# Kernel optimization log

Measured on AMD Instinct MI355X. Metric: run time of the kernel, lower is better.

## Reference

```python
import jax, jax.numpy as jnp
import numpy as np

B, T, C, H = 2, 2048, 1024, 16
HD = C // H  # head dim = 64


def setup_inputs() -> dict:
    key = jax.random.key(0)
    k0, k1, k2 = jax.random.split(key, 3)
    x = jax.random.normal(k0, (B, T, C), jnp.float32)
    W_attn = jax.random.normal(k1, (C, 3 * C), jnp.float32) * 0.02
    b_attn = jnp.zeros((3 * C,), jnp.float32)
    W_proj = jax.random.normal(k2, (C, C), jnp.float32) * 0.02
    b_proj = jnp.zeros((C,), jnp.float32)
    # rope: (1,1,T,HD//2,2,2) stack of 2x2 rotation matrices [[cos,-sin],[sin,cos]]
    inv_freq = 1.0 / (10000.0 ** (jnp.arange(0, HD, 2, dtype=jnp.float32) / HD))
    ang = jnp.arange(T, dtype=jnp.float32)[:, None] * inv_freq[None, :]  # (T, HD//2)
    cos, sin = jnp.cos(ang), jnp.sin(ang)
    rope = jnp.stack([jnp.stack([cos, -sin], -1), jnp.stack([sin, cos], -1)], -2)
    rope = rope[None, None]  # (1,1,T,HD//2,2,2)
    return dict(x=x, W_attn=W_attn, b_attn=b_attn, W_proj=W_proj, b_proj=b_proj, rope=rope)


def reference(x, W_attn, b_attn, W_proj, b_proj, rope):
    Bv, Tv, Cv = x.shape
    Hd = Cv // H
    qkv = x @ W_attn + b_attn                      # (B,T,3C) fused QKV proj
    q, k, v = jnp.split(qkv, 3, axis=-1)

    def heads(t):
        return t.reshape(Bv, Tv, H, Hd).transpose(0, 2, 1, 3)  # (B,H,T,Hd)

    q, k, v = heads(q), heads(k), heads(v)

    cos = rope[..., 0, 0][..., None]               # (1,1,T,Hd//2,1)
    sin = rope[..., 1, 0][..., None]

    def rot(t):
        tr = t.reshape(Bv, H, Tv, Hd // 2, 2)
        xr, yr = tr[..., 0:1], tr[..., 1:2]
        out = jnp.concatenate([xr * cos - yr * sin, xr * sin + yr * cos], axis=-1)
        return out.reshape(Bv, H, Tv, Hd)

    q, k = rot(q), rot(k)

    scale = 1.0 / np.sqrt(Hd).astype(np.float32)
    att = jnp.einsum('bhqd,bhkd->bhqk', q, k) * scale
    mask = jnp.tril(jnp.ones((Tv, Tv), dtype=bool))  # causal
    att = jnp.where(mask[None, None], att, -jnp.inf)
    att = jax.nn.softmax(att, axis=-1)
    y = jnp.einsum('bhqk,bhkd->bhqd', att, v)
    y = y.transpose(0, 2, 1, 3).reshape(Bv, Tv, Cv)
    return y @ W_proj + b_proj
```

## Files before the change

kernel.cpp:

```cpp
#include <hip/hip_runtime.h>
#include <hip/hip_bf16.h>

typedef __attribute__((ext_vector_type(8))) short short8;
typedef __attribute__((ext_vector_type(4))) short short4b;
typedef __attribute__((ext_vector_type(4))) float f32x4;
typedef __attribute__((ext_vector_type(16))) float f32x16;
typedef __attribute__((ext_vector_type(4))) unsigned u32x4;

static constexpr int Bb = 2, Tt = 2048, Cc = 1024, Hh = 16;
static constexpr int BT = Bb * Tt;
static constexpr int N1 = 3 * Cc;

__device__ __forceinline__ unsigned short f2b(float f) {
  union { float f; unsigned u; } v; v.f = f;
  unsigned r = v.u + 0x7fffu + ((v.u >> 16) & 1u);
  return (unsigned short)(r >> 16);
}
__device__ __forceinline__ float b2f(short s) {
  union { unsigned u; float f; } v; v.u = ((unsigned)(unsigned short)s) << 16;
  return v.f;
}

__global__ __launch_bounds__(256) void k_cast(const float* __restrict__ in,
                                              unsigned short* __restrict__ out, int n) {
  int i = (blockIdx.x * 256 + threadIdx.x) * 8;
  if (i >= n) return;
  float4 a = *reinterpret_cast<const float4*>(in + i);
  float4 b = *reinterpret_cast<const float4*>(in + i + 4);
  short8 o;
  o[0] = f2b(a.x); o[1] = f2b(a.y); o[2] = f2b(a.z); o[3] = f2b(a.w);
  o[4] = f2b(b.x); o[5] = f2b(b.y); o[6] = f2b(b.z); o[7] = f2b(b.w);
  *reinterpret_cast<short8*>(out + i) = o;
}

__global__ __launch_bounds__(256) void k_tcast(const float* __restrict__ in,
                                               unsigned short* __restrict__ out,
                                               int R, int Ccol) {
  __shared__ float tile[32][33];
  int cb = blockIdx.x * 32, rb = blockIdx.y * 32;
  int tx = threadIdx.x & 31, ty = threadIdx.x >> 5;
  for (int i = 0; i < 32; i += 8)
    tile[ty + i][tx] = in[(size_t)(rb + ty + i) * Ccol + cb + tx];
  __syncthreads();
  for (int i = 0; i < 32; i += 8)
    out[(size_t)(cb + ty + i) * R + rb + tx] = f2b(tile[tx][ty + i]);
}

template <int NF, int OUT_BF16>
__global__ __launch_bounds__(512, 2)
void k_gemm8(const unsigned short* __restrict__ A, const unsigned short* __restrict__ Bt,
             const float* __restrict__ bias, void* __restrict__ Cout,
             int M, int N, int K) {
  constexpr int BN = NF * 64;
  constexpr int ASZ = 256 * 64;
  constexpr int BSZ = BN * 64;
  constexpr int STRIDE = ASZ + BSZ;
  extern __shared__ unsigned short lds[];
  const int tid = threadIdx.x, lane = tid & 63, w = tid >> 6;
  const int wm = w >> 2, wn = w & 3;
  const int l15 = lane & 15, l4 = lane >> 4;
  int nbx = gridDim.x;
  int lin = blockIdx.y * nbx + blockIdx.x;
  int cpx = (nbx * gridDim.y) >> 3;
  lin = (lin & 7) * cpx + (lin >> 3);
  const int mb = lin / nbx, nb = lin % nbx;
  const size_t arow0 = (size_t)mb * 256;
  const size_t brow0 = (size_t)nb * BN;

  const int srow = lane >> 3;
  const int scol = (((lane & 7) * 16) ^ (srow << 4)) >> 1;
  auto stage = [&](int buf, int k0) {
    unsigned short* Ab = lds + buf * STRIDE;
    unsigned short* Bb = Ab + ASZ;
#pragma unroll
    for (int i = 0; i < 4; i++) {
      int c = w + 8 * i;
      const unsigned short* g = A + (arow0 + c * 8 + srow) * (size_t)K + k0 + scol;
      __builtin_amdgcn_global_load_lds((const __attribute__((address_space(1))) void*)g,
          (__attribute__((address_space(3))) void*)(Ab + c * 512), 16, 0, 0);
    }
#pragma unroll
    for (int i = 0; i < NF; i++) {
      int c = w + 8 * i;
      const unsigned short* g = Bt + (brow0 + c * 8 + srow) * (size_t)K + k0 + scol;
      __builtin_amdgcn_global_load_lds((const __attribute__((address_space(1))) void*)g,
          (__attribute__((address_space(3))) void*)(Bb + c * 512), 16, 0, 0);
    }
  };

  f32x4 acc[8][NF] = {};
  const int NK = K >> 6;

  stage(0, 0);
  asm volatile("s_waitcnt vmcnt(0)" ::: "memory");
  asm volatile("s_barrier" ::: "memory");

  for (int kt = 0; kt < NK; kt++) {
    int buf = kt & 1;
    if (kt + 1 < NK) stage(buf ^ 1, (kt + 1) << 6);
    const unsigned short* Ab = lds + buf * STRIDE;
    const unsigned short* Bb = Ab + ASZ;
    short8 af[8][2];
#pragma unroll
    for (int p = 0; p < NF; p++) {
      if (p == 0) {
#pragma unroll
        for (int m = 0; m < 8; m++) {
          int ra = wm * 128 + m * 16 + l15;
#pragma unroll
          for (int kk = 0; kk < 2; kk++) {
            int cb = (kk * 64 + l4 * 16) ^ ((ra & 7) << 4);
            af[m][kk] = *reinterpret_cast<const short8*>(Ab + ra * 64 + (cb >> 1));
          }
        }
      }
      short8 bfr[2];
      int rb = wn * (NF * 16) + p * 16 + l15;
#pragma unroll
      for (int kk = 0; kk < 2; kk++) {
        int cb = (kk * 64 + l4 * 16) ^ ((rb & 7) << 4);
        bfr[kk] = *reinterpret_cast<const short8*>(Bb + rb * 64 + (cb >> 1));
      }
      asm volatile("s_barrier" ::: "memory");
      asm volatile("s_waitcnt lgkmcnt(0)" ::: "memory");
      __builtin_amdgcn_sched_barrier(0);
      __builtin_amdgcn_s_setprio(1);
#pragma unroll
      for (int m = 0; m < 8; m++) {
        acc[m][p] = __builtin_amdgcn_mfma_f32_16x16x32_bf16(af[m][0], bfr[0], acc[m][p], 0, 0, 0);
        acc[m][p] = __builtin_amdgcn_mfma_f32_16x16x32_bf16(af[m][1], bfr[1], acc[m][p], 0, 0, 0);
      }
      __builtin_amdgcn_s_setprio(0);
      if (p == NF - 1)
        asm volatile("s_waitcnt vmcnt(0)" ::: "memory");
      asm volatile("s_barrier" ::: "memory");
    }
  }

#pragma unroll
  for (int m = 0; m < 8; m++) {
#pragma unroll
    for (int n = 0; n < NF; n++) {
      int ccol = nb * BN + wn * (NF * 16) + n * 16 + l15;
      float bv = bias[ccol];
#pragma unroll
      for (int j = 0; j < 4; j++) {
        int r = mb * 256 + wm * 128 + m * 16 + l4 * 4 + j;
        float v = acc[m][n][j] + bv;
        if (OUT_BF16)
          ((unsigned short*)Cout)[(size_t)r * N + ccol] = f2b(v);
        else
          ((float*)Cout)[(size_t)r * N + ccol] = v;
      }
    }
  }
}

__global__ __launch_bounds__(256)
void k_rope(const unsigned short* __restrict__ qkv, const float* __restrict__ rope,
            unsigned short* __restrict__ Qs, unsigned short* __restrict__ Ks,
            unsigned short* __restrict__ Vt) {
  __shared__ unsigned short vt_l[64][72];
  const float QS = 0.125f * 1.44269504f;
  int bid = blockIdx.x;
  int tb = bid & 31, h = (bid >> 5) & 15, b = bid >> 9;
  int tid = threadIdx.x;
#pragma unroll
  for (int r = 0; r < 2; r++) {
    int e = (r * 256 + tid) * 8;
    int tl = e >> 6, d = e & 63;
    int t = tb * 64 + tl;
    const unsigned short* rowp = qkv + (size_t)(b * Tt + t) * 3072 + h * 64 + d;
    short8 qv = *reinterpret_cast<const short8*>(rowp);
    short8 kv = *reinterpret_cast<const short8*>(rowp + 1024);
    short8 vv = *reinterpret_cast<const short8*>(rowp + 2048);
    short8 qo, ko;
#pragma unroll
    for (int p = 0; p < 4; p++) {
      int j = (d >> 1) + p;
      float4 rv = *reinterpret_cast<const float4*>(rope + ((size_t)t * 32 + j) * 4);
      float xq = b2f(qv[2 * p]), yq = b2f(qv[2 * p + 1]);
      float xk = b2f(kv[2 * p]), yk = b2f(kv[2 * p + 1]);
      qo[2 * p]     = (short)f2b((xq * rv.x + yq * rv.y) * QS);
      qo[2 * p + 1] = (short)f2b((xq * rv.z + yq * rv.w) * QS);
      ko[2 * p]     = (short)f2b(xk * rv.x + yk * rv.y);
      ko[2 * p + 1] = (short)f2b(xk * rv.z + yk * rv.w);
    }
    size_t qdst = ((size_t)(b * 16 + h) * Tt + t) * 64 + d;
    *reinterpret_cast<short8*>(Qs + qdst) = qo;
    *reinterpret_cast<short8*>(Ks + qdst) = ko;
#pragma unroll
    for (int i2 = 0; i2 < 8; i2++) vt_l[d + i2][tl] = (unsigned short)vv[i2];
  }
  __syncthreads();
#pragma unroll
  for (int r = 0; r < 2; r++) {
    int e = (r * 256 + tid) * 8;
    int dl = e >> 6, tl = e & 63;
    short8 o = *reinterpret_cast<const short8*>(&vt_l[dl][tl]);
    *reinterpret_cast<short8*>(Vt + ((size_t)(b * 16 + h) * 64 + dl) * Tt + tb * 64 + tl) = o;
  }
}

__device__ __forceinline__ float tmax16(const f32x16& v) {
  float a0 = fmaxf(v[0], v[1]),   a1 = fmaxf(v[2], v[3]);
  float a2 = fmaxf(v[4], v[5]),   a3 = fmaxf(v[6], v[7]);
  float a4 = fmaxf(v[8], v[9]),   a5 = fmaxf(v[10], v[11]);
  float a6 = fmaxf(v[12], v[13]), a7 = fmaxf(v[14], v[15]);
  float b0 = fmaxf(a0, a1), b1 = fmaxf(a2, a3), b2 = fmaxf(a4, a5), b3 = fmaxf(a6, a7);
  return fmaxf(fmaxf(b0, b1), fmaxf(b2, b3));
}

template <bool DIAG>
__device__ __forceinline__ void attn_tile128(
    const unsigned short* Kl, const unsigned short* Vl,
    int w, int l31, int hi, const short8 qf[4],
    float& m_run, float& l_run, f32x16 oacc[2]) {
  const int ktmax = DIAG ? w : 3;
  f32x16 s[4];
#pragma unroll
  for (int kt = 0; kt < 4; kt++) {
    if (kt > ktmax) continue;
    f32x16 acc = {};
    int rk = kt * 32 + l31;
    int sw = (rk & 7) << 4;
    const unsigned short* krow = Kl + rk * 64;
#pragma unroll
    for (int kk = 0; kk < 4; kk++) {
      short8 kf = *reinterpret_cast<const short8*>(krow + (((kk * 32 + hi * 16) ^ sw) >> 1));
      acc = __builtin_amdgcn_mfma_f32_32x32x16_bf16(kf, qf[kk], acc, 0, 0, 0);
    }
    if (DIAG && kt == w) {
#pragma unroll
      for (int r = 0; r < 16; r++) {
        int e = (r & 3) + 8 * (r >> 2) + 4 * hi;
        if (e > l31) acc[r] = -1e30f;
      }
    }
    s[kt] = acc;
  }
  float km[4];
#pragma unroll
  for (int kt = 0; kt < 4; kt++) km[kt] = (kt <= ktmax) ? tmax16(s[kt]) : -1e30f;
  float mx = fmaxf(fmaxf(km[0], km[1]), fmaxf(km[2], km[3]));
  mx = fmaxf(mx, __shfl_xor(mx, 32));
  float nm = fmaxf(m_run, mx);
  float fsc = __builtin_amdgcn_exp2f(m_run - nm);
  m_run = nm;
#pragma unroll
  for (int dt = 0; dt < 2; dt++)
#pragma unroll
    for (int r = 0; r < 16; r++) oacc[dt][r] *= fsc;

  float kps[4] = {0.f, 0.f, 0.f, 0.f};
#pragma unroll
  for (int kt = 0; kt < 4; kt++) {
    if (kt > ktmax) continue;
    float p[16];
#pragma unroll
    for (int r = 0; r < 16; r++) p[r] = __builtin_amdgcn_exp2f(s[kt][r] - nm);
    float s0 = (p[0] + p[1]) + (p[2] + p[3]);
    float s1 = (p[4] + p[5]) + (p[6] + p[7]);
    float s2 = (p[8] + p[9]) + (p[10] + p[11]);
    float s3 = (p[12] + p[13]) + (p[14] + p[15]);
    kps[kt] = (s0 + s1) + (s2 + s3);
    unsigned P[8];
#pragma unroll
    for (int i = 0; i < 8; i++) {
      unsigned lo = (__builtin_bit_cast(unsigned, p[2 * i]) + 0x8000u) >> 16;
      unsigned h2 = (__builtin_bit_cast(unsigned, p[2 * i + 1]) + 0x8000u) & 0xffff0000u;
      P[i] = lo | h2;
    }
    unsigned Y0 = (unsigned)__shfl_xor((int)(hi ? P[0] : P[2]), 32);
    unsigned Y1 = (unsigned)__shfl_xor((int)(hi ? P[1] : P[3]), 32);
    unsigned Y2 = (unsigned)__shfl_xor((int)(hi ? P[4] : P[6]), 32);
    unsigned Y3 = (unsigned)__shfl_xor((int)(hi ? P[5] : P[7]), 32);
    u32x4 c0 = hi ? u32x4{Y0, Y1, P[2], P[3]} : u32x4{P[0], P[1], Y0, Y1};
    u32x4 c1 = hi ? u32x4{Y2, Y3, P[6], P[7]} : u32x4{P[4], P[5], Y2, Y3};
    short8 pf0 = __builtin_bit_cast(short8, c0);
    short8 pf1 = __builtin_bit_cast(short8, c1);
#pragma unroll
    for (int dt = 0; dt < 2; dt++) {
      int d = dt * 32 + l31;
      int sv = (d & 15) << 4;
      const unsigned short* vrow = Vl + d * 128;
      short8 vf0 = *reinterpret_cast<const short8*>(vrow + (((kt * 64 + hi * 16) ^ sv) >> 1));
      short8 vf1 = *reinterpret_cast<const short8*>(vrow + (((kt * 64 + 32 + hi * 16) ^ sv) >> 1));
      oacc[dt] = __builtin_amdgcn_mfma_f32_32x32x16_bf16(vf0, pf0, oacc[dt], 0, 0, 0);
      oacc[dt] = __builtin_amdgcn_mfma_f32_32x32x16_bf16(vf1, pf1, oacc[dt], 0, 0, 0);
    }
  }
  float psum = (kps[0] + kps[1]) + (kps[2] + kps[3]);
  psum += __shfl_xor(psum, 32);
  l_run = l_run * fsc + psum;
}

__global__ __launch_bounds__(256)
void k_attn(const unsigned short* __restrict__ Qs, const unsigned short* __restrict__ Ks,
            const unsigned short* __restrict__ Vt, unsigned short* __restrict__ Y) {
  __shared__ unsigned short lds[32768];
  int tid = threadIdx.x, lane = tid & 63, w = tid >> 6;
  int s = blockIdx.x;
  int half = s >> 8;
  int p = s & 255;
  int bh = p >> 3;
  int j = p & 7;
  int qb = half ? j : 15 - j;
  int b = bh >> 4, h = bh & 15;
  int l31 = lane & 31, hi = lane >> 5;
  int qw0 = qb * 128 + w * 32;
  const unsigned short* Qb = Qs + (size_t)bh * Tt * 64;
  const unsigned short* Kb = Ks + (size_t)bh * Tt * 64;
  const unsigned short* Vb = Vt + (size_t)bh * 64 * Tt;

  auto stage = [&](int buf, int kv0) {
    unsigned short* Kbuf = lds + buf * 8192;
    unsigned short* Vbuf = lds + 16384 + buf * 8192;
    int krow = lane >> 3;
    int kcolb = ((lane & 7) * 16) ^ ((krow & 7) << 4);
#pragma unroll
    for (int cc = 0; cc < 4; cc++) {
      int c = w + cc * 4;
      const unsigned short* gk = Kb + (size_t)(kv0 + c * 8 + krow) * 64 + (kcolb >> 1);
      __builtin_amdgcn_global_load_lds((const __attribute__((address_space(1))) void*)gk,
          (__attribute__((address_space(3))) void*)(Kbuf + c * 512), 16, 0, 0);
      int vr = c * 4 + (lane >> 4);
      int vcolb = ((lane & 15) * 16) ^ ((vr & 15) << 4);
      const unsigned short* gv = Vb + (size_t)vr * Tt + kv0 + (vcolb >> 1);
      __builtin_amdgcn_global_load_lds((const __attribute__((address_space(1))) void*)gv,
          (__attribute__((address_space(3))) void*)(Vbuf + c * 512), 16, 0, 0);
    }
  };

  short8 qf[4];
#pragma unroll
  for (int kk = 0; kk < 4; kk++)
    qf[kk] = *reinterpret_cast<const short8*>(Qb + (size_t)(qw0 + l31) * 64 + kk * 16 + hi * 8);

  float m_run = -1e30f, l_run = 0.f;
  f32x16 oacc[2] = {};
  const int nt = qb + 1;

  stage(0, 0);
  __syncthreads();
  int cur = 0;
  for (int it = 0; it < nt - 1; ++it) {
    stage(cur ^ 1, (it + 1) * 128);
    attn_tile128<false>(lds + cur * 8192, lds + 16384 + cur * 8192,
                        w, l31, hi, qf, m_run, l_run, oacc);
    __syncthreads();
    cur ^= 1;
  }
  attn_tile128<true>(lds + cur * 8192, lds + 16384 + cur * 8192,
                     w, l31, hi, qf, m_run, l_run, oacc);

  float inv = 1.0f / l_run;
  int t = qw0 + l31;
  unsigned short* yrow = Y + ((size_t)b * Tt + t) * Cc + h * 64;
#pragma unroll
  for (int dt = 0; dt < 2; dt++)
#pragma unroll
    for (int q4 = 0; q4 < 4; q4++) {
      short4b o;
#pragma unroll
      for (int jj = 0; jj < 4; jj++) o[jj] = (short)f2b(oacc[dt][q4 * 4 + jj] * inv);
      *reinterpret_cast<short4b*>(yrow + dt * 32 + q4 * 8 + hi * 4) = o;
    }
}

extern "C" void kernel_launch(void* const* d_in, const int* in_sizes, int n_in,
                              void* d_out, int out_size, void* d_ws, size_t ws_size,
                              hipStream_t stream) {
  (void)in_sizes; (void)n_in; (void)out_size; (void)ws_size;
  const float* x      = (const float*)d_in[0];
  const float* W_attn = (const float*)d_in[1];
  const float* b_attn = (const float*)d_in[2];
  const float* W_proj = (const float*)d_in[3];
  const float* b_proj = (const float*)d_in[4];
  const float* rope   = (const float*)d_in[5];
  float* out = (float*)d_out;

  char* ws = (char*)d_ws;
  unsigned short* xb  = (unsigned short*)(ws);
  unsigned short* WaT = (unsigned short*)(ws + (8u << 20));
  unsigned short* WpT = (unsigned short*)(ws + (14u << 20));
  unsigned short* qkv = (unsigned short*)(ws + (16u << 20));
  unsigned short* Qs  = (unsigned short*)(ws + (40u << 20));
  unsigned short* Ks  = (unsigned short*)(ws + (48u << 20));
  unsigned short* Vt  = (unsigned short*)(ws + (56u << 20));
  unsigned short* Yb  = (unsigned short*)(ws + (64u << 20));

  constexpr int LDS_QKV  = (256 + 192) * 64 * 2 * 2;
  constexpr int LDS_PROJ = (256 + 128) * 64 * 2 * 2;
  (void)hipFuncSetAttribute(reinterpret_cast<const void*>(&k_gemm8<3, 1>),
                            hipFuncAttributeMaxDynamicSharedMemorySize, LDS_QKV);
  (void)hipFuncSetAttribute(reinterpret_cast<const void*>(&k_gemm8<2, 0>),
                            hipFuncAttributeMaxDynamicSharedMemorySize, LDS_PROJ);

  k_cast<<<2048, 256, 0, stream>>>(x, xb, BT * Cc);
  k_tcast<<<dim3(N1 / 32, Cc / 32), 256, 0, stream>>>(W_attn, WaT, Cc, N1);
  k_tcast<<<dim3(Cc / 32, Cc / 32), 256, 0, stream>>>(W_proj, WpT, Cc, Cc);
  k_gemm8<3, 1><<<dim3(N1 / 192, BT / 256), 512, LDS_QKV, stream>>>(xb, WaT, b_attn, qkv, BT, N1, Cc);
  k_rope<<<Bb * Hh * (Tt / 64), 256, 0, stream>>>(qkv, rope, Qs, Ks, Vt);
  k_attn<<<Bb * Hh * (Tt / 128), 256, 0, stream>>>(Qs, Ks, Vt, Yb);
  k_gemm8<2, 0><<<dim3(Cc / 128, BT / 256), 512, LDS_PROJ, stream>>>(Yb, WpT, b_proj, out, BT, Cc, Cc);
}
```

Before: 121.9 us.

## Fuse RoPE, scaling and head scatter into QKV GEMM epilogue; remap attention blocks per XCD

Removes the separate rope kernel and the intermediate qkv buffer. The QKV GEMM epilogue now applies bias, RoPE (pairing lanes via shuffle) and the softmax scale, then writes Q/K in head-major layout and V transposed. This avoids a full round trip of the qkv tensor through memory and one launch, at the cost of scattered 2-byte stores in the epilogue. Attention block indexing is also remapped so each XCD handles a fixed set of heads, with a heavy-first causal ordering, to improve L2 locality.

```diff
diff --git a/kernel.cpp b/kernel.cpp
--- a/kernel.cpp
+++ b/kernel.cpp
@@ -10,6 +10,7 @@
 static constexpr int Bb = 2, Tt = 2048, Cc = 1024, Hh = 16;
 static constexpr int BT = Bb * Tt;
 static constexpr int N1 = 3 * Cc;
+static constexpr float QS = 0.125f * 1.44269504f;
 
 __device__ __forceinline__ unsigned short f2b(float f) {
   union { float f; unsigned u; } v; v.f = f;
@@ -46,10 +47,12 @@
     out[(size_t)(cb + ty + i) * R + rb + tx] = f2b(tile[tx][ty + i]);
 }
 
-template <int NF, int OUT_BF16>
+template <int NF, int EPI>
 __global__ __launch_bounds__(512, 2)
 void k_gemm8(const unsigned short* __restrict__ A, const unsigned short* __restrict__ Bt,
              const float* __restrict__ bias, void* __restrict__ Cout,
+             const float* __restrict__ rope, unsigned short* __restrict__ Qs,
+             unsigned short* __restrict__ Ks, unsigned short* __restrict__ Vt,
              int M, int N, int K) {
   constexpr int BN = NF * 64;
   constexpr int ASZ = 256 * 64;
@@ -141,64 +144,45 @@
   for (int m = 0; m < 8; m++) {
 #pragma unroll
     for (int n = 0; n < NF; n++) {
-      int ccol = nb * BN + wn * (NF * 16) + n * 16 + l15;
-      float bv = bias[ccol];
-#pragma unroll
-      for (int j = 0; j < 4; j++) {
-        int r = mb * 256 + wm * 128 + m * 16 + l4 * 4 + j;
-        float v = acc[m][n][j] + bv;
-        if (OUT_BF16)
-          ((unsigned short*)Cout)[(size_t)r * N + ccol] = f2b(v);
-        else
-          ((float*)Cout)[(size_t)r * N + ccol] = v;
-      }
-    }
-  }
-}
-
-__global__ __launch_bounds__(256)
-void k_rope(const unsigned short* __restrict__ qkv, const float* __restrict__ rope,
-            unsigned short* __restrict__ Qs, unsigned short* __restrict__ Ks,
-            unsigned short* __restrict__ Vt) {
-  __shared__ unsigned short vt_l[64][72];
-  const float QS = 0.125f * 1.44269504f;
-  int bid = blockIdx.x;
-  int tb = bid & 31, h = (bid >> 5) & 15, b = bid >> 9;
-  int tid = threadIdx.x;
-#pragma unroll
-  for (int r = 0; r < 2; r++) {
-    int e = (r * 256 + tid) * 8;
-    int tl = e >> 6, d = e & 63;
-    int t = tb * 64 + tl;
-    const unsigned short* rowp = qkv + (size_t)(b * Tt + t) * 3072 + h * 64 + d;
-    short8 qv = *reinterpret_cast<const short8*>(rowp);
-    short8 kv = *reinterpret_cast<const short8*>(rowp + 1024);
-    short8 vv = *reinterpret_cast<const short8*>(rowp + 2048);
-    short8 qo, ko;
-#pragma unroll
-    for (int p = 0; p < 4; p++) {
-      int j = (d >> 1) + p;
-      float4 rv = *reinterpret_cast<const float4*>(rope + ((size_t)t * 32 + j) * 4);
-      float xq = b2f(qv[2 * p]), yq = b2f(qv[2 * p + 1]);
-      float xk = b2f(kv[2 * p]), yk = b2f(kv[2 * p + 1]);
-      qo[2 * p]     = (short)f2b((xq * rv.x + yq * rv.y) * QS);
-      qo[2 * p + 1] = (short)f2b((xq * rv.z + yq * rv.w) * QS);
-      ko[2 * p]     = (short)f2b(xk * rv.x + yk * rv.y);
-      ko[2 * p + 1] = (short)f2b(xk * rv.z + yk * rv.w);
-    }
-    size_t qdst = ((size_t)(b * 16 + h) * Tt + t) * 64 + d;
-    *reinterpret_cast<short8*>(Qs + qdst) = qo;
-    *reinterpret_cast<short8*>(Ks + qdst) = ko;
-#pragma unroll
-    for (int i2 = 0; i2 < 8; i2++) vt_l[d + i2][tl] = (unsigned short)vv[i2];
-  }
-  __syncthreads();
-#pragma unroll
-  for (int r = 0; r < 2; r++) {
-    int e = (r * 256 + tid) * 8;
-    int dl = e >> 6, tl = e & 63;
-    short8 o = *reinterpret_cast<const short8*>(&vt_l[dl][tl]);
-    *reinterpret_cast<short8*>(Vt + ((size_t)(b * 16 + h) * 64 + dl) * Tt + tb * 64 + tl) = o;
+      int ccol0 = nb * BN + wn * (NF * 16) + n * 16;
+      float bv = bias[ccol0 + l15];
+      int r0 = mb * 256 + wm * 128 + m * 16 + l4 * 4;
+      if (EPI == 0) {
+#pragma unroll
+        for (int j = 0; j < 4; j++)
+          ((float*)Cout)[(size_t)(r0 + j) * N + ccol0 + l15] = acc[m][n][j] + bv;
+      } else {
+        int cls = ccol0 >> 10;
+        int h = (ccol0 >> 6) & 15;
+        int d = (ccol0 & 63) + l15;
+        int bq = r0 >> 11;
+        int t0 = r0 & 2047;
+        size_t bh = (size_t)bq * 16 + h;
+        if (cls == 2) {
+          short4b o;
+#pragma unroll
+          for (int j = 0; j < 4; j++) o[j] = (short)f2b(acc[m][n][j] + bv);
+          *reinterpret_cast<short4b*>(Vt + (bh * 64 + d) * Tt + t0) = o;
+        } else {
+          unsigned short* dst = (cls == 0) ? Qs : Ks;
+          int jj = d >> 1;
+          int odd = d & 1;
+#pragma unroll
+          for (int j = 0; j < 4; j++) {
+            float v = acc[m][n][j] + bv;
+            float part = __shfl_xor(v, 1);
+            float2 sc = *reinterpret_cast<const float2*>(
+                rope + (size_t)(t0 + j) * 128 + jj * 4 + 2);
+            float x = odd ? part : v;
+            float y = odd ? v : part;
+            float rot = odd ? (x * sc.x + y * sc.y)
+                            : (x * sc.y - y * sc.x);
+            if (cls == 0) rot *= QS;
+            dst[(bh * Tt + (t0 + j)) * 64 + d] = f2b(rot);
+          }
+        }
+      }
+    }
   }
 }
 
@@ -301,11 +285,10 @@
   __shared__ unsigned short lds[32768];
   int tid = threadIdx.x, lane = tid & 63, w = tid >> 6;
   int s = blockIdx.x;
-  int half = s >> 8;
-  int p = s & 255;
-  int bh = p >> 3;
-  int j = p & 7;
-  int qb = half ? j : 15 - j;
+  int xcd = s & 7;
+  int o = s >> 3;
+  int bh = xcd * 4 + (o & 3);
+  int qb = (o < 32) ? (15 - (o >> 2)) : ((o - 32) >> 2);
   int b = bh >> 4, h = bh & 15;
   int l31 = lane & 31, hi = lane >> 5;
   int qw0 = qb * 128 + w * 32;
@@ -361,10 +344,10 @@
   for (int dt = 0; dt < 2; dt++)
 #pragma unroll
     for (int q4 = 0; q4 < 4; q4++) {
-      short4b o;
-#pragma unroll
-      for (int jj = 0; jj < 4; jj++) o[jj] = (short)f2b(oacc[dt][q4 * 4 + jj] * inv);
-      *reinterpret_cast<short4b*>(yrow + dt * 32 + q4 * 8 + hi * 4) = o;
+      short4b oo;
+#pragma unroll
+      for (int jj = 0; jj < 4; jj++) oo[jj] = (short)f2b(oacc[dt][q4 * 4 + jj] * inv);
+      *reinterpret_cast<short4b*>(yrow + dt * 32 + q4 * 8 + hi * 4) = oo;
     }
 }
 
@@ -384,11 +367,10 @@
   unsigned short* xb  = (unsigned short*)(ws);
   unsigned short* WaT = (unsigned short*)(ws + (8u << 20));
   unsigned short* WpT = (unsigned short*)(ws + (14u << 20));
-  unsigned short* qkv = (unsigned short*)(ws + (16u << 20));
-  unsigned short* Qs  = (unsigned short*)(ws + (40u << 20));
-  unsigned short* Ks  = (unsigned short*)(ws + (48u << 20));
-  unsigned short* Vt  = (unsigned short*)(ws + (56u << 20));
-  unsigned short* Yb  = (unsigned short*)(ws + (64u << 20));
+  unsigned short* Qs  = (unsigned short*)(ws + (16u << 20));
+  unsigned short* Ks  = (unsigned short*)(ws + (24u << 20));
+  unsigned short* Vt  = (unsigned short*)(ws + (32u << 20));
+  unsigned short* Yb  = (unsigned short*)(ws + (40u << 20));
 
   constexpr int LDS_QKV  = (256 + 192) * 64 * 2 * 2;
   constexpr int LDS_PROJ = (256 + 128) * 64 * 2 * 2;
@@ -400,8 +382,9 @@
   k_cast<<<2048, 256, 0, stream>>>(x, xb, BT * Cc);
   k_tcast<<<dim3(N1 / 32, Cc / 32), 256, 0, stream>>>(W_attn, WaT, Cc, N1);
   k_tcast<<<dim3(Cc / 32, Cc / 32), 256, 0, stream>>>(W_proj, WpT, Cc, Cc);
-  k_gemm8<3, 1><<<dim3(N1 / 192, BT / 256), 512, LDS_QKV, stream>>>(xb, WaT, b_attn, qkv, BT, N1, Cc);
-  k_rope<<<Bb * Hh * (Tt / 64), 256, 0, stream>>>(qkv, rope, Qs, Ks, Vt);
+  k_gemm8<3, 1><<<dim3(N1 / 192, BT / 256), 512, LDS_QKV, stream>>>(
+      xb, WaT, b_attn, nullptr, rope, Qs, Ks, Vt, BT, N1, Cc);
   k_attn<<<Bb * Hh * (Tt / 128), 256, 0, stream>>>(Qs, Ks, Vt, Yb);
-  k_gemm8<2, 0><<<dim3(Cc / 128, BT / 256), 512, LDS_PROJ, stream>>>(Yb, WpT, b_proj, out, BT, Cc, Cc);
-}
+  k_gemm8<2, 0><<<dim3(Cc / 128, BT / 256), 512, LDS_PROJ, stream>>>(
+      Yb, WpT, b_proj, out, nullptr, nullptr, nullptr, nullptr, BT, Cc, Cc);
+}
```

Result: slower. 128.6 us (+5.4%).
